# Optimization experiments

Measured on AMD Instinct MI355X. Metric: run time of the kernel, lower is better.

## Reference

```python
import jax, jax.numpy as jnp
import numpy as np

B, S, D, H = 4, 2048, 1024, 16
HD = D // H


def setup_inputs() -> dict:
    key = jax.random.key(0)
    ks = jax.random.split(key, 12)
    scale = 1.0 / np.sqrt(D)
    inp = {
        "query": jax.random.normal(ks[0], (B, S, D), jnp.float32),
        "key": jax.random.normal(ks[1], (B, S, D), jnp.float32),
        "value": jax.random.normal(ks[2], (B, S, D), jnp.float32),
        "mask": jax.random.randint(ks[3], (B, 1, S, S), 0, 2).astype(jnp.float32),
        "Wq": jax.random.normal(ks[4], (D, D), jnp.float32) * scale,
        "bq": jnp.zeros((D,), jnp.float32),
        "Wk": jax.random.normal(ks[5], (D, D), jnp.float32) * scale,
        "bk": jnp.zeros((D,), jnp.float32),
        "Wv": jax.random.normal(ks[6], (D, D), jnp.float32) * scale,
        "bv": jnp.zeros((D,), jnp.float32),
        "Wo": jax.random.normal(ks[7], (D, D), jnp.float32) * scale,
        "bo": jnp.zeros((D,), jnp.float32),
    }
    return inp


def reference(query, key, value, mask, Wq, bq, Wk, bk, Wv, bv, Wo, bo):
    # projections, then split heads: [B, S, D] -> [B, H, S, HD]
    def split_heads(x):
        return x.reshape(B, S, H, HD).transpose(0, 2, 1, 3)

    q = split_heads(query @ Wq + bq)
    k = split_heads(key @ Wk + bk)
    v = split_heads(value @ Wv + bv)

    # scores [B, H, Sq, Sk]
    logits = jnp.einsum("bhqd,bhkd->bhqk", q, k) / jnp.sqrt(jnp.float32(HD))
    logits = logits + mask * (-1e9)
    attn = jax.nn.softmax(logits, axis=-1)
    out = jnp.einsum("bhqk,bhkd->bhqd", attn, v)  # [B, H, Sq, HD]
    out = out.transpose(0, 2, 1, 3).reshape(B, S, D)
    return out @ Wo + bo
```

## Files before the change

### kernel.cpp

```cpp
#include <hip/hip_runtime.h>

#define DI __device__ __forceinline__

typedef __attribute__((ext_vector_type(8))) short short8v;
typedef __attribute__((ext_vector_type(4))) float f32x4;

static constexpr int B_ = 4, S_ = 2048, D_ = 1024, H_ = 16, HD_ = 64;
static constexpr int M_ = B_ * S_;

DI unsigned short f2bf(float f) {
  unsigned u = __builtin_bit_cast(unsigned, f);
  u = (u + 0x7fffu + ((u >> 16) & 1u)) >> 16;
  return (unsigned short)u;
}

DI unsigned cvt_pk_bf16(float lo, float hi) {
  unsigned r;
  asm("v_cvt_pk_bf16_f32 %0, %1, %2" : "=v"(r) : "v"(lo), "v"(hi));
  return r;
}

DI void async_copy16(const void* g, void* l) {
  __builtin_amdgcn_global_load_lds((const __attribute__((address_space(1))) void*)g,
                                   (__attribute__((address_space(3))) void*)l, 16, 0, 0);
}

__global__ __launch_bounds__(256) void cast_bf16_kernel(const float* __restrict__ in,
                                                        unsigned short* __restrict__ out,
                                                        int n4) {
  int i = blockIdx.x * blockDim.x + threadIdx.x;
  int stride = gridDim.x * blockDim.x;
  for (; i < n4; i += stride) {
    float4 v = reinterpret_cast<const float4*>(in)[i];
    ushort4 o;
    o.x = f2bf(v.x); o.y = f2bf(v.y); o.z = f2bf(v.z); o.w = f2bf(v.w);
    reinterpret_cast<ushort4*>(out)[i] = o;
  }
}

__global__ __launch_bounds__(256) void transpose_cast_kernel(const float* __restrict__ W,
                                                             unsigned short* __restrict__ Wt,
                                                             int n) {
  __shared__ float t[32][33];
  int bx = blockIdx.x * 32, by = blockIdx.y * 32;
  int x = threadIdx.x, y0 = threadIdx.y;
#pragma unroll
  for (int yy = 0; yy < 32; yy += 8)
    t[y0 + yy][x] = W[(long)(by + y0 + yy) * n + bx + x];
  __syncthreads();
#pragma unroll
  for (int yy = 0; yy < 32; yy += 8)
    Wt[(long)(bx + y0 + yy) * n + by + x] = f2bf(t[x][y0 + yy]);
}

__global__ __launch_bounds__(256) void pack_mask_kernel(const float* __restrict__ mask,
                                                        unsigned long long* __restrict__ bits,
                                                        int nwords) {
  int lane = threadIdx.x & 63;
  int wpb = blockDim.x >> 6;
  int w = blockIdx.x * wpb + (threadIdx.x >> 6);
  int stride = gridDim.x * wpb;
  for (; w < nwords; w += stride) {
    float v = mask[(long)w * 64 + lane];
    unsigned long long b = __ballot(v > 0.5f);
    if (lane == 0) {
      int bb = w >> 16, q = (w >> 5) & 2047, kt64 = w & 31;
      bits[((long)bb << 16) | (kt64 << 11) | q] = b;
    }
  }
}

template <int MODE>
__global__ __launch_bounds__(256) void gemm_bt_kernel(const unsigned short* __restrict__ A,
                                                      const unsigned short* __restrict__ Bt,
                                                      const float* __restrict__ bias,
                                                      void* __restrict__ out,
                                                      int Mdim, int Ndim, int Kdim, float scale) {
  __shared__ unsigned short As[2][128 * 32];
  __shared__ unsigned short Bs[2][128 * 32];
  const int tid = threadIdx.x;
  const int lane = tid & 63;
  const int w = tid >> 6;
  const int g = lane >> 4;
  const int l15 = lane & 15;
  const int bm = blockIdx.x * 128;
  const int bn = blockIdx.y * 128;
  const int wr = w >> 1, wc = w & 1;

  f32x4 zero = {0.f, 0.f, 0.f, 0.f};
  f32x4 acc[4][4];
#pragma unroll
  for (int i = 0; i < 4; ++i)
#pragma unroll
    for (int j = 0; j < 4; ++j) acc[i][j] = zero;

  const int srow = lane >> 2;
  const int scol = (lane & 3) * 8;

  auto stageg = [&](int k0, int bi) {
#pragma unroll
    for (int i = 0; i < 2; ++i) {
      int q = w * 2 + i;
      int row = q * 16 + srow;
      async_copy16(&A[(long)(bm + row) * Kdim + k0 + scol], &As[bi][q * 512]);
      async_copy16(&Bt[(long)(bn + row) * Kdim + k0 + scol], &Bs[bi][q * 512]);
    }
  };

  stageg(0, 0);
  asm volatile("s_waitcnt vmcnt(0)" ::: "memory");
  __builtin_amdgcn_sched_barrier(0);
  __builtin_amdgcn_s_barrier();
  asm volatile("" ::: "memory");

  const int NT = Kdim / 32;
  int cur = 0;
  for (int t = 0; t < NT; ++t) {
    if (t + 1 < NT) stageg((t + 1) * 32, cur ^ 1);

    short8v a[4], b[4];
#pragma unroll
    for (int i = 0; i < 4; ++i)
      a[i] = *reinterpret_cast<const short8v*>(&As[cur][(wr * 64 + i * 16 + l15) * 32 + g * 8]);
#pragma unroll
    for (int j = 0; j < 4; ++j)
      b[j] = *reinterpret_cast<const short8v*>(&Bs[cur][(wc * 64 + j * 16 + l15) * 32 + g * 8]);
#pragma unroll
    for (int i = 0; i < 4; ++i)
#pragma unroll
      for (int j = 0; j < 4; ++j)
        acc[i][j] = __builtin_amdgcn_mfma_f32_16x16x32_bf16(a[i], b[j], acc[i][j], 0, 0, 0);

    asm volatile("s_waitcnt vmcnt(0) lgkmcnt(0)" ::: "memory");
    __builtin_amdgcn_sched_barrier(0);
    __builtin_amdgcn_s_barrier();
    asm volatile("" ::: "memory");
    cur ^= 1;
  }

#pragma unroll
  for (int jj = 0; jj < 4; ++jj) {
    int n = bn + wc * 64 + jj * 16 + l15;
    float bs = bias[n];
#pragma unroll
    for (int i = 0; i < 4; ++i) {
      int m0 = bm + wr * 64 + i * 16 + g * 4;
      if (MODE == 0) {
        unsigned short* o = (unsigned short*)out;
#pragma unroll
        for (int r = 0; r < 4; ++r)
          o[(long)(m0 + r) * Ndim + n] = f2bf((acc[i][jj][r] + bs) * scale);
      } else if (MODE == 1) {
        int b2 = m0 >> 11, s0 = m0 & 2047;
        int s0p = (s0 & ~31) | (((s0 >> 2) & 3) << 3) | (((s0 >> 4) & 1) << 2);
        int h2 = n >> 6, d2 = n & 63;
        unsigned short* o = (unsigned short*)out;
        ushort4 v;
        v.x = f2bf(acc[i][jj][0] + bs);
        v.y = f2bf(acc[i][jj][1] + bs);
        v.z = f2bf(acc[i][jj][2] + bs);
        v.w = f2bf(acc[i][jj][3] + bs);
        *reinterpret_cast<ushort4*>(&o[((long)((b2 * 16 + h2) * 64 + d2) << 11) + s0p]) = v;
      } else {
        float* o = (float*)out;
#pragma unroll
        for (int r = 0; r < 4; ++r)
          o[(long)(m0 + r) * Ndim + n] = acc[i][jj][r] + bs;
      }
    }
  }
}

__global__ __launch_bounds__(256, 2) void attn_kernel(const unsigned short* __restrict__ Q,
                                                      const unsigned short* __restrict__ Kb,
                                                      const unsigned short* __restrict__ Vt,
                                                      const unsigned long long* __restrict__ mbits,
                                                      unsigned short* __restrict__ attn) {
  __shared__ unsigned short Ks[2][64 * 64];
  __shared__ unsigned short Vs[2][64 * 64];
  const int lane = threadIdx.x & 63;
  const int w = threadIdx.x >> 6;
  const int g = lane >> 4;
  const int l15 = lane & 15;
  const int qt = blockIdx.x;
  const int bh = blockIdx.y;
  const int b = bh >> 4, h = bh & 15;
  const int q0 = qt * 128 + w * 32 + l15;

  const unsigned short* qp = Q + ((long)b * S_ + q0) * D_ + h * HD_ + g * 8;
  short8v qfr[2][2];
  qfr[0][0] = *reinterpret_cast<const short8v*>(qp);
  qfr[0][1] = *reinterpret_cast<const short8v*>(qp + 32);
  qfr[1][0] = *reinterpret_cast<const short8v*>(qp + 16 * D_);
  qfr[1][1] = *reinterpret_cast<const short8v*>(qp + 16 * D_ + 32);

  const int srow = lane >> 3;
  const int schunk = ((lane & 7) ^ (lane >> 3)) * 8;
  const unsigned short* kstage = Kb + (long)b * S_ * D_ + h * HD_;
  const unsigned short* vstage = Vt + (long)bh * HD_ * S_;

  f32x4 zero = {0.f, 0.f, 0.f, 0.f};
  f32x4 oacc[2][4];
#pragma unroll
  for (int qf = 0; qf < 2; ++qf)
#pragma unroll
    for (int d = 0; d < 4; ++d) oacc[qf][d] = zero;
  float m_run[2] = {-1e30f, -1e30f}, l_run[2] = {0.f, 0.f};

  const unsigned long long* mbase = mbits + ((long)b << 16);
  const int swz = l15 & 7;

  auto stage = [&](int kt, int bi) {
#pragma unroll
    for (int i = 0; i < 2; ++i) {
      int blk8 = w * 2 + i;
      async_copy16(&kstage[(long)(kt + blk8 * 8 + srow) * D_ + schunk], &Ks[bi][blk8 * 512]);
      async_copy16(&vstage[(long)(blk8 * 8 + srow) * S_ + kt + schunk], &Vs[bi][blk8 * 512]);
    }
  };

  unsigned long long mw_cur0 = mbase[q0];
  unsigned long long mw_cur1 = mbase[q0 + 16];
  stage(0, 0);

  int cur = 0;
  for (int t = 0; t < S_ / 64; ++t) {
    unsigned long long mw_nxt0 = 0, mw_nxt1 = 0;
    if (t < S_ / 64 - 1) {
      mw_nxt0 = mbase[((t + 1) << 11) + q0];
      mw_nxt1 = mbase[((t + 1) << 11) + q0 + 16];
      stage((t + 1) * 64, cur ^ 1);
      asm volatile("s_waitcnt vmcnt(6)" ::: "memory");
    } else {
      asm volatile("s_waitcnt vmcnt(0)" ::: "memory");
    }
    __builtin_amdgcn_s_barrier();
    asm volatile("" ::: "memory");

    const unsigned short* Kbuf = &Ks[cur][0];
    const unsigned short* Vbuf = &Vs[cur][0];

    f32x4 lt[2][4];
#pragma unroll
    for (int g2 = 0; g2 < 4; ++g2) {
      const unsigned short* kr = &Kbuf[(g2 * 16 + l15) * 64];
      short8v kf0 = *reinterpret_cast<const short8v*>(&kr[(g ^ swz) * 8]);
      short8v kf1 = *reinterpret_cast<const short8v*>(&kr[((g + 4) ^ swz) * 8]);
#pragma unroll
      for (int qf = 0; qf < 2; ++qf) {
        f32x4 c = zero;
        c = __builtin_amdgcn_mfma_f32_16x16x32_bf16(kf0, qfr[qf][0], c, 0, 0, 0);
        c = __builtin_amdgcn_mfma_f32_16x16x32_bf16(kf1, qfr[qf][1], c, 0, 0, 0);
        lt[qf][g2] = c;
      }
    }

    short8v pfr[2][2];
#pragma unroll
    for (int qf = 0; qf < 2; ++qf) {
      unsigned long long mw = qf ? mw_cur1 : mw_cur0;
      float tmax = -1e30f;
#pragma unroll
      for (int g2 = 0; g2 < 4; ++g2)
#pragma unroll
        for (int r = 0; r < 4; ++r) {
          int krel = g2 * 16 + g * 4 + r;
          float v = ((mw >> krel) & 1ull) ? -1e30f : lt[qf][g2][r];
          lt[qf][g2][r] = v;
          tmax = fmaxf(tmax, v);
        }
      tmax = fmaxf(tmax, __shfl_xor(tmax, 16));
      tmax = fmaxf(tmax, __shfl_xor(tmax, 32));
      float m_new = fmaxf(m_run[qf], tmax);
      float alpha = __builtin_amdgcn_exp2f(m_run[qf] - m_new);
      float p[4][4];
      float tsum = 0.f;
#pragma unroll
      for (int g2 = 0; g2 < 4; ++g2)
#pragma unroll
        for (int r = 0; r < 4; ++r) {
          p[g2][r] = __builtin_amdgcn_exp2f(lt[qf][g2][r] - m_new);
          tsum += p[g2][r];
        }
      tsum += __shfl_xor(tsum, 16);
      tsum += __shfl_xor(tsum, 32);
      l_run[qf] = l_run[qf] * alpha + tsum;
      m_run[qf] = m_new;
#pragma unroll
      for (int d = 0; d < 4; ++d) oacc[qf][d] *= alpha;
#pragma unroll
      for (int s = 0; s < 2; ++s) {
        union { unsigned u[4]; short8v v; } pu;
        pu.u[0] = cvt_pk_bf16(p[2 * s][0], p[2 * s][1]);
        pu.u[1] = cvt_pk_bf16(p[2 * s][2], p[2 * s][3]);
        pu.u[2] = cvt_pk_bf16(p[2 * s + 1][0], p[2 * s + 1][1]);
        pu.u[3] = cvt_pk_bf16(p[2 * s + 1][2], p[2 * s + 1][3]);
        pfr[qf][s] = pu.v;
      }
    }

#pragma unroll
    for (int d0 = 0; d0 < 4; ++d0) {
      const unsigned short* vr = &Vbuf[(d0 * 16 + l15) * 64];
#pragma unroll
      for (int s = 0; s < 2; ++s) {
        short8v vf = *reinterpret_cast<const short8v*>(&vr[((s * 4 + g) ^ swz) * 8]);
#pragma unroll
        for (int qf = 0; qf < 2; ++qf)
          oacc[qf][d0] = __builtin_amdgcn_mfma_f32_16x16x32_bf16(vf, pfr[qf][s], oacc[qf][d0], 0, 0, 0);
      }
    }

    asm volatile("" ::: "memory");
    __builtin_amdgcn_s_barrier();
    asm volatile("" ::: "memory");
    mw_cur0 = mw_nxt0;
    mw_cur1 = mw_nxt1;
    cur ^= 1;
  }

#pragma unroll
  for (int qf = 0; qf < 2; ++qf) {
    float inv = 1.f / l_run[qf];
    int q = q0 + qf * 16;
#pragma unroll
    for (int d0 = 0; d0 < 4; ++d0) {
      ushort4 o;
      o.x = f2bf(oacc[qf][d0][0] * inv);
      o.y = f2bf(oacc[qf][d0][1] * inv);
      o.z = f2bf(oacc[qf][d0][2] * inv);
      o.w = f2bf(oacc[qf][d0][3] * inv);
      *reinterpret_cast<ushort4*>(&attn[((long)b * S_ + q) * D_ + h * HD_ + d0 * 16 + g * 4]) = o;
    }
  }
}

extern "C" void kernel_launch(void* const* d_in, const int* in_sizes, int n_in,
                              void* d_out, int out_size, void* d_ws, size_t ws_size,
                              hipStream_t stream) {
  const float* query = (const float*)d_in[0];
  const float* key   = (const float*)d_in[1];
  const float* value = (const float*)d_in[2];
  const float* mask  = (const float*)d_in[3];
  const float* Wq = (const float*)d_in[4];
  const float* bq = (const float*)d_in[5];
  const float* Wk = (const float*)d_in[6];
  const float* bk = (const float*)d_in[7];
  const float* Wv = (const float*)d_in[8];
  const float* bv = (const float*)d_in[9];
  const float* Wo = (const float*)d_in[10];
  const float* bo = (const float*)d_in[11];

  char* ws = (char*)d_ws;
  unsigned short* XQ  = (unsigned short*)(ws);
  unsigned short* XK  = (unsigned short*)(ws + (16ull << 20));
  unsigned short* XV  = (unsigned short*)(ws + (32ull << 20));
  unsigned short* WQT = (unsigned short*)(ws + (48ull << 20));
  unsigned short* WKT = (unsigned short*)(ws + (50ull << 20));
  unsigned short* WVT = (unsigned short*)(ws + (52ull << 20));
  unsigned short* WOT = (unsigned short*)(ws + (54ull << 20));
  unsigned short* QB  = (unsigned short*)(ws + (56ull << 20));
  unsigned short* KB  = (unsigned short*)(ws + (72ull << 20));
  unsigned short* VT  = (unsigned short*)(ws + (88ull << 20));
  unsigned long long* MBITS = (unsigned long long*)(ws + (16ull << 20));
  unsigned short* ATTN = XQ;

  const int n4 = M_ * D_ / 4;
  cast_bf16_kernel<<<2048, 256, 0, stream>>>(query, XQ, n4);
  cast_bf16_kernel<<<2048, 256, 0, stream>>>(key,   XK, n4);
  cast_bf16_kernel<<<2048, 256, 0, stream>>>(value, XV, n4);

  dim3 tg(D_ / 32, D_ / 32), tb(32, 8);
  transpose_cast_kernel<<<tg, tb, 0, stream>>>(Wq, WQT, D_);
  transpose_cast_kernel<<<tg, tb, 0, stream>>>(Wk, WKT, D_);
  transpose_cast_kernel<<<tg, tb, 0, stream>>>(Wv, WVT, D_);
  transpose_cast_kernel<<<tg, tb, 0, stream>>>(Wo, WOT, D_);

  dim3 gg(M_ / 128, D_ / 128);
  gemm_bt_kernel<0><<<gg, 256, 0, stream>>>(XQ, WQT, bq, QB, M_, D_, D_, 0.18033688011112042f);
  gemm_bt_kernel<0><<<gg, 256, 0, stream>>>(XK, WKT, bk, KB, M_, D_, D_, 1.f);
  gemm_bt_kernel<1><<<gg, 256, 0, stream>>>(XV, WVT, bv, VT, M_, D_, D_, 1.f);

  pack_mask_kernel<<<2048, 256, 0, stream>>>(mask, MBITS, B_ * S_ * S_ / 64);

  dim3 ag(S_ / 128, B_ * H_);
  attn_kernel<<<ag, 256, 0, stream>>>(QB, KB, VT, MBITS, ATTN);

  gemm_bt_kernel<2><<<gg, 256, 0, stream>>>(ATTN, WOT, bo, d_out, M_, D_, D_, 1.f);
}
```

Measured before the change: 309.7 us.

## Halve attention query tile per block to raise occupancy and add MFMA priority

Each wave of the attention kernel now handles 16 query rows instead of 32, so a block covers 64 queries and the grid doubles. Launch bounds rise from 2 to 4 blocks per CU, and the waitcnt is adjusted to the one remaining mask load. s_setprio raises wave priority around the MFMA sections. The aim is more resident waves to hide latency, at the cost of twice as much K/V staging traffic per query and less reuse of each K/V fragment loaded from LDS.

```diff
diff --git a/kernel.cpp b/kernel.cpp
--- a/kernel.cpp
+++ b/kernel.cpp
@@ -171,7 +171,7 @@
   }
 }
 
-__global__ __launch_bounds__(256, 2) void attn_kernel(const unsigned short* __restrict__ Q,
+__global__ __launch_bounds__(256, 4) void attn_kernel(const unsigned short* __restrict__ Q,
                                                       const unsigned short* __restrict__ Kb,
                                                       const unsigned short* __restrict__ Vt,
                                                       const unsigned long long* __restrict__ mbits,
@@ -185,14 +185,11 @@
   const int qt = blockIdx.x;
   const int bh = blockIdx.y;
   const int b = bh >> 4, h = bh & 15;
-  const int q0 = qt * 128 + w * 32 + l15;
+  const int q0 = qt * 64 + w * 16 + l15;
 
   const unsigned short* qp = Q + ((long)b * S_ + q0) * D_ + h * HD_ + g * 8;
-  short8v qfr[2][2];
-  qfr[0][0] = *reinterpret_cast<const short8v*>(qp);
-  qfr[0][1] = *reinterpret_cast<const short8v*>(qp + 32);
-  qfr[1][0] = *reinterpret_cast<const short8v*>(qp + 16 * D_);
-  qfr[1][1] = *reinterpret_cast<const short8v*>(qp + 16 * D_ + 32);
+  short8v qf0 = *reinterpret_cast<const short8v*>(qp);
+  short8v qf1 = *reinterpret_cast<const short8v*>(qp + 32);
 
   const int srow = lane >> 3;
   const int schunk = ((lane & 7) ^ (lane >> 3)) * 8;
@@ -200,12 +197,8 @@
   const unsigned short* vstage = Vt + (long)bh * HD_ * S_;
 
   f32x4 zero = {0.f, 0.f, 0.f, 0.f};
-  f32x4 oacc[2][4];
-#pragma unroll
-  for (int qf = 0; qf < 2; ++qf)
-#pragma unroll
-    for (int d = 0; d < 4; ++d) oacc[qf][d] = zero;
-  float m_run[2] = {-1e30f, -1e30f}, l_run[2] = {0.f, 0.f};
+  f32x4 oacc[4] = {zero, zero, zero, zero};
+  float m_run = -1e30f, l_run = 0.f;
 
   const unsigned long long* mbase = mbits + ((long)b << 16);
   const int swz = l15 & 7;
@@ -219,18 +212,16 @@
     }
   };
 
-  unsigned long long mw_cur0 = mbase[q0];
-  unsigned long long mw_cur1 = mbase[q0 + 16];
+  unsigned long long mw_cur = mbase[q0];
   stage(0, 0);
 
   int cur = 0;
   for (int t = 0; t < S_ / 64; ++t) {
-    unsigned long long mw_nxt0 = 0, mw_nxt1 = 0;
+    unsigned long long mw_nxt = 0;
     if (t < S_ / 64 - 1) {
-      mw_nxt0 = mbase[((t + 1) << 11) + q0];
-      mw_nxt1 = mbase[((t + 1) << 11) + q0 + 16];
+      mw_nxt = mbase[((t + 1) << 11) + q0];
       stage((t + 1) * 64, cur ^ 1);
-      asm volatile("s_waitcnt vmcnt(6)" ::: "memory");
+      asm volatile("s_waitcnt vmcnt(5)" ::: "memory");
     } else {
       asm volatile("s_waitcnt vmcnt(0)" ::: "memory");
     }
@@ -240,98 +231,88 @@
     const unsigned short* Kbuf = &Ks[cur][0];
     const unsigned short* Vbuf = &Vs[cur][0];
 
-    f32x4 lt[2][4];
+    f32x4 lt[4];
+    __builtin_amdgcn_s_setprio(1);
 #pragma unroll
     for (int g2 = 0; g2 < 4; ++g2) {
       const unsigned short* kr = &Kbuf[(g2 * 16 + l15) * 64];
       short8v kf0 = *reinterpret_cast<const short8v*>(&kr[(g ^ swz) * 8]);
       short8v kf1 = *reinterpret_cast<const short8v*>(&kr[((g + 4) ^ swz) * 8]);
-#pragma unroll
-      for (int qf = 0; qf < 2; ++qf) {
-        f32x4 c = zero;
-        c = __builtin_amdgcn_mfma_f32_16x16x32_bf16(kf0, qfr[qf][0], c, 0, 0, 0);
-        c = __builtin_amdgcn_mfma_f32_16x16x32_bf16(kf1, qfr[qf][1], c, 0, 0, 0);
-        lt[qf][g2] = c;
+      f32x4 c = zero;
+      c = __builtin_amdgcn_mfma_f32_16x16x32_bf16(kf0, qf0, c, 0, 0, 0);
+      c = __builtin_amdgcn_mfma_f32_16x16x32_bf16(kf1, qf1, c, 0, 0, 0);
+      lt[g2] = c;
+    }
+    __builtin_amdgcn_s_setprio(0);
+
+    float tmax = -1e30f;
+#pragma unroll
+    for (int g2 = 0; g2 < 4; ++g2)
+#pragma unroll
+      for (int r = 0; r < 4; ++r) {
+        int krel = g2 * 16 + g * 4 + r;
+        float v = ((mw_cur >> krel) & 1ull) ? -1e30f : lt[g2][r];
+        lt[g2][r] = v;
+        tmax = fmaxf(tmax, v);
       }
-    }
-
-    short8v pfr[2][2];
-#pragma unroll
-    for (int qf = 0; qf < 2; ++qf) {
-      unsigned long long mw = qf ? mw_cur1 : mw_cur0;
-      float tmax = -1e30f;
-#pragma unroll
-      for (int g2 = 0; g2 < 4; ++g2)
-#pragma unroll
-        for (int r = 0; r < 4; ++r) {
-          int krel = g2 * 16 + g * 4 + r;
-          float v = ((mw >> krel) & 1ull) ? -1e30f : lt[qf][g2][r];
-          lt[qf][g2][r] = v;
-          tmax = fmaxf(tmax, v);
-        }
-      tmax = fmaxf(tmax, __shfl_xor(tmax, 16));
-      tmax = fmaxf(tmax, __shfl_xor(tmax, 32));
-      float m_new = fmaxf(m_run[qf], tmax);
-      float alpha = __builtin_amdgcn_exp2f(m_run[qf] - m_new);
-      float p[4][4];
-      float tsum = 0.f;
-#pragma unroll
-      for (int g2 = 0; g2 < 4; ++g2)
-#pragma unroll
-        for (int r = 0; r < 4; ++r) {
-          p[g2][r] = __builtin_amdgcn_exp2f(lt[qf][g2][r] - m_new);
-          tsum += p[g2][r];
-        }
-      tsum += __shfl_xor(tsum, 16);
-      tsum += __shfl_xor(tsum, 32);
-      l_run[qf] = l_run[qf] * alpha + tsum;
-      m_run[qf] = m_new;
-#pragma unroll
-      for (int d = 0; d < 4; ++d) oacc[qf][d] *= alpha;
-#pragma unroll
-      for (int s = 0; s < 2; ++s) {
-        union { unsigned u[4]; short8v v; } pu;
-        pu.u[0] = cvt_pk_bf16(p[2 * s][0], p[2 * s][1]);
-        pu.u[1] = cvt_pk_bf16(p[2 * s][2], p[2 * s][3]);
-        pu.u[2] = cvt_pk_bf16(p[2 * s + 1][0], p[2 * s + 1][1]);
-        pu.u[3] = cvt_pk_bf16(p[2 * s + 1][2], p[2 * s + 1][3]);
-        pfr[qf][s] = pu.v;
+    tmax = fmaxf(tmax, __shfl_xor(tmax, 16));
+    tmax = fmaxf(tmax, __shfl_xor(tmax, 32));
+    float m_new = fmaxf(m_run, tmax);
+    float alpha = __builtin_amdgcn_exp2f(m_run - m_new);
+    float p[4][4];
+    float tsum = 0.f;
+#pragma unroll
+    for (int g2 = 0; g2 < 4; ++g2)
+#pragma unroll
+      for (int r = 0; r < 4; ++r) {
+        p[g2][r] = __builtin_amdgcn_exp2f(lt[g2][r] - m_new);
+        tsum += p[g2][r];
       }
-    }
-
+    tsum += __shfl_xor(tsum, 16);
+    tsum += __shfl_xor(tsum, 32);
+    l_run = l_run * alpha + tsum;
+    m_run = m_new;
+#pragma unroll
+    for (int d = 0; d < 4; ++d) oacc[d] *= alpha;
+    short8v pfr[2];
+#pragma unroll
+    for (int s = 0; s < 2; ++s) {
+      union { unsigned u[4]; short8v v; } pu;
+      pu.u[0] = cvt_pk_bf16(p[2 * s][0], p[2 * s][1]);
+      pu.u[1] = cvt_pk_bf16(p[2 * s][2], p[2 * s][3]);
+      pu.u[2] = cvt_pk_bf16(p[2 * s + 1][0], p[2 * s + 1][1]);
+      pu.u[3] = cvt_pk_bf16(p[2 * s + 1][2], p[2 * s + 1][3]);
+      pfr[s] = pu.v;
+    }
+
+    __builtin_amdgcn_s_setprio(1);
 #pragma unroll
     for (int d0 = 0; d0 < 4; ++d0) {
       const unsigned short* vr = &Vbuf[(d0 * 16 + l15) * 64];
 #pragma unroll
       for (int s = 0; s < 2; ++s) {
         short8v vf = *reinterpret_cast<const short8v*>(&vr[((s * 4 + g) ^ swz) * 8]);
-#pragma unroll
-        for (int qf = 0; qf < 2; ++qf)
-          oacc[qf][d0] = __builtin_amdgcn_mfma_f32_16x16x32_bf16(vf, pfr[qf][s], oacc[qf][d0], 0, 0, 0);
+        oacc[d0] = __builtin_amdgcn_mfma_f32_16x16x32_bf16(vf, pfr[s], oacc[d0], 0, 0, 0);
       }
     }
+    __builtin_amdgcn_s_setprio(0);
 
     asm volatile("" ::: "memory");
     __builtin_amdgcn_s_barrier();
     asm volatile("" ::: "memory");
-    mw_cur0 = mw_nxt0;
-    mw_cur1 = mw_nxt1;
+    mw_cur = mw_nxt;
     cur ^= 1;
   }
 
-#pragma unroll
-  for (int qf = 0; qf < 2; ++qf) {
-    float inv = 1.f / l_run[qf];
-    int q = q0 + qf * 16;
-#pragma unroll
-    for (int d0 = 0; d0 < 4; ++d0) {
-      ushort4 o;
-      o.x = f2bf(oacc[qf][d0][0] * inv);
-      o.y = f2bf(oacc[qf][d0][1] * inv);
-      o.z = f2bf(oacc[qf][d0][2] * inv);
-      o.w = f2bf(oacc[qf][d0][3] * inv);
-      *reinterpret_cast<ushort4*>(&attn[((long)b * S_ + q) * D_ + h * HD_ + d0 * 16 + g * 4]) = o;
-    }
+  float inv = 1.f / l_run;
+#pragma unroll
+  for (int d0 = 0; d0 < 4; ++d0) {
+    ushort4 o;
+    o.x = f2bf(oacc[d0][0] * inv);
+    o.y = f2bf(oacc[d0][1] * inv);
+    o.z = f2bf(oacc[d0][2] * inv);
+    o.w = f2bf(oacc[d0][3] * inv);
+    *reinterpret_cast<ushort4*>(&attn[((long)b * S_ + q0) * D_ + h * HD_ + d0 * 16 + g * 4]) = o;
   }
 }
 
@@ -383,7 +364,7 @@
 
   pack_mask_kernel<<<2048, 256, 0, stream>>>(mask, MBITS, B_ * S_ * S_ / 64);
 
-  dim3 ag(S_ / 128, B_ * H_);
+  dim3 ag(S_ / 64, B_ * H_);
   attn_kernel<<<ag, 256, 0, stream>>>(QB, KB, VT, MBITS, ATTN);
 
   gemm_bt_kernel<2><<<gg, 256, 0, stream>>>(ATTN, WOT, bo, d_out, M_, D_, D_, 1.f);
```

Measured after the change: 308.3 us. About the same (-0.5%).
